# Kernel tuning notes

Hardware: AMD Instinct MI355X
Metric: run time of the kernel (lower is better)

The kernel has to match this reference:

```python
import jax, jax.numpy as jnp
import numpy as np

N_HEAD = 16


def setup_inputs() -> dict:
    key = jax.random.key(0)
    k1, k2, k3 = jax.random.split(key, 3)
    B, T, C = 2, 2048, 1024
    x = jax.random.normal(k1, (B, T, C), dtype=jnp.float32)
    Wqkv = jax.random.normal(k2, (C, 3 * C), dtype=jnp.float32) * 0.02
    bqkv = jnp.zeros((3 * C,), dtype=jnp.float32)
    Wproj = jax.random.normal(k3, (C, C), dtype=jnp.float32) * 0.02
    bproj = jnp.zeros((C,), dtype=jnp.float32)
    return {"x": x, "Wqkv": Wqkv, "bqkv": bqkv, "Wproj": Wproj, "bproj": bproj}


def reference(x, Wqkv, bqkv, Wproj, bproj):
    b, t, c = x.shape
    h = N_HEAD
    d = c // h  # head_dim
    # qkv projection, split into q,k,v per head: (b,t,3,h,d)
    qkv = (x @ Wqkv + bqkv).reshape(b, t, 3, h, d)
    q, k, v = qkv[:, :, 0], qkv[:, :, 1], qkv[:, :, 2]  # each (b,t,h,d)
    # Faithful quirk of original: n_state = head_dim // heads, scale = 1/sqrt(n_state)
    scale = jnp.float32(1.0 / np.sqrt(d // h))
    # attn_mode == 'all': dense non-causal attention
    w = jnp.einsum('bqhd,bkhd->bhqk', q, k)  # (b,h,t,t)
    w = jax.nn.softmax(w * scale, axis=-1)
    a = jnp.einsum('bhqk,bkhd->bqhd', w, v).reshape(b, t, c)
    return a @ Wproj + bproj
```

## Files before the change

### kernel.cpp

```cpp
#include <hip/hip_runtime.h>

typedef float floatx4 __attribute__((ext_vector_type(4)));
typedef float floatx16 __attribute__((ext_vector_type(16)));
typedef __bf16 bf16x8 __attribute__((ext_vector_type(8)));
typedef __bf16 bf16x4 __attribute__((ext_vector_type(4)));
typedef __bf16 bf16x2 __attribute__((ext_vector_type(2)));
typedef float floatx2 __attribute__((ext_vector_type(2)));

#define MFMA16 __builtin_amdgcn_mfma_f32_16x16x32_bf16
#define MFMA32 __builtin_amdgcn_mfma_f32_32x32x16_bf16

typedef const __attribute__((address_space(1))) void* gas_t;
typedef __attribute__((address_space(3))) void* las_t;
#define GLD16(g, l) __builtin_amdgcn_global_load_lds((gas_t)(g), (las_t)(l), 16, 0, 0)

static __device__ __forceinline__ unsigned short f2bf(float f) {
  union { float f; unsigned int u; } v; v.f = f;
  unsigned int r = v.u + 0x7fffu + ((v.u >> 16) & 1u);
  return (unsigned short)(r >> 16);
}

static __device__ __forceinline__ unsigned pk2(float a, float b) {
  floatx2 v; v[0] = a; v[1] = b;
  union { bf16x2 h; unsigned u; } u;
  u.h = __builtin_convertvector(v, bf16x2);
  return u.u;
}

static __device__ __forceinline__ void cast_transpose_tile(
    const float* __restrict__ in, unsigned short* __restrict__ out,
    int R, int C, int bx, int by) {
  const int r0 = by * 64, c0 = bx * 64;
  const int tid = threadIdx.x;
  __shared__ float tl[64][65];
  const int rr = tid >> 4, cc = (tid & 15) * 4;
#pragma unroll
  for (int i = 0; i < 4; ++i) {
    int row = rr + i * 16;
    float4 v = *(const float4*)(in + (size_t)(r0 + row) * C + c0 + cc);
    tl[row][cc] = v.x; tl[row][cc + 1] = v.y;
    tl[row][cc + 2] = v.z; tl[row][cc + 3] = v.w;
  }
  __syncthreads();
  const int cl = tid >> 2, rbase = (tid & 3) * 16;
  unsigned short o[16];
#pragma unroll
  for (int j = 0; j < 16; ++j) o[j] = f2bf(tl[rbase + j][cl]);
  unsigned short* dst = out + (size_t)(c0 + cl) * R + r0 + rbase;
  *(uint4*)dst = *(uint4*)o;
  *(uint4*)(dst + 8) = *(uint4*)(o + 8);
}

__global__ __launch_bounds__(256) void prologue_kernel(
    const float* __restrict__ x, unsigned short* __restrict__ Xb,
    const float* __restrict__ Wqkv, unsigned short* __restrict__ Wqkvt,
    const float* __restrict__ Wproj, unsigned short* __restrict__ Wprojt) {
  const int bid = blockIdx.x;
  if (bid < 4096) {
    int i = bid * 256 + threadIdx.x;
    float4 v = ((const float4*)x)[i];
    ushort4 o;
    o.x = f2bf(v.x); o.y = f2bf(v.y); o.z = f2bf(v.z); o.w = f2bf(v.w);
    ((ushort4*)Xb)[i] = o;
  } else if (bid < 4096 + 768) {
    int b2 = bid - 4096;
    cast_transpose_tile(Wqkv, Wqkvt, 1024, 3072, b2 % 48, b2 / 48);
  } else {
    int b3 = bid - 4096 - 768;
    cast_transpose_tile(Wproj, Wprojt, 1024, 1024, b3 % 16, b3 / 16);
  }
}

__global__ __launch_bounds__(256) void gemm_qkv(
    const unsigned short* __restrict__ A,
    const unsigned short* __restrict__ Bt,
    const float* __restrict__ bias,
    unsigned short* __restrict__ Q,
    unsigned short* __restrict__ Kc,
    unsigned short* __restrict__ Vt) {
  const int K = 1024;
  const int m0 = blockIdx.y * 128, n0 = blockIdx.x * 128;
  const int tid = threadIdx.x, w = tid >> 6, l = tid & 63;
  const int l16 = l & 15, lq = l >> 4;
  const int wm = w >> 1, wn = w & 1;
  const int which = n0 >> 10;

  __shared__ __align__(16) unsigned short SH[32768];

  floatx4 acc[4][4] = {};

  int sA[4], sB[4];
  unsigned ldso[4];
#pragma unroll
  for (int j = 0; j < 4; ++j) {
    int s = j * 256 + tid;
    int row = s >> 3, blk = (s & 7) ^ (row & 7);
    sA[j] = (m0 + row) * K + blk * 8;
    sB[j] = (n0 + row) * K + blk * 8;
    ldso[j] = (unsigned)(j * 256 + w * 64) * 8;
  }

#pragma unroll
  for (int j = 0; j < 4; ++j) {
    GLD16(A + sA[j], SH + ldso[j]);
    GLD16(Bt + sB[j], SH + 8192 + ldso[j]);
  }

  if (which == 2) {
    for (int k0 = 0; k0 < K; k0 += 64) {
      __syncthreads();
      const int cur = (k0 >> 6) & 1;
      if (k0 + 64 < K) {
        const int nxt = cur ^ 1;
#pragma unroll
        for (int j = 0; j < 4; ++j) {
          GLD16(A + sA[j] + k0 + 64, SH + nxt * 16384 + ldso[j]);
          GLD16(Bt + sB[j] + k0 + 64, SH + nxt * 16384 + 8192 + ldso[j]);
        }
      }
      const unsigned short* As = SH + cur * 16384;
      const unsigned short* Bs = SH + cur * 16384 + 8192;
#pragma unroll
      for (int kk = 0; kk < 2; ++kk) {
        bf16x8 af[4], bf[4];
#pragma unroll
        for (int mi = 0; mi < 4; ++mi) {
          int row = wm * 64 + mi * 16 + l16;
          int blk = (kk * 4 + lq) ^ (l16 & 7);
          af[mi] = *(const bf16x8*)(As + row * 64 + blk * 8);
        }
#pragma unroll
        for (int ni = 0; ni < 4; ++ni) {
          int row = wn * 64 + ni * 16 + l16;
          int blk = (kk * 4 + lq) ^ (l16 & 7);
          bf[ni] = *(const bf16x8*)(Bs + row * 64 + blk * 8);
        }
#pragma unroll
        for (int ni = 0; ni < 4; ++ni)
#pragma unroll
          for (int mi = 0; mi < 4; ++mi)
            acc[mi][ni] = MFMA16(af[mi], bf[ni], acc[mi][ni], 0, 0, 0);
      }
    }
    float bv[4];
#pragma unroll
    for (int ni = 0; ni < 4; ++ni) bv[ni] = bias[n0 + wn * 64 + ni * 16 + l16];
    __syncthreads();
    unsigned short* E = SH + w * 2304;
    const int bh = (m0 >> 11) * 16 + ((n0 & 1023) >> 6) + wn;
    const int tt0 = (m0 & 2047) + wm * 64;
    const int m8 = l & 7, bc = 16 * (m8 >> 1) + 4 * (m8 & 1);
#pragma unroll
    for (int p = 0; p < 2; ++p) {
#pragma unroll
      for (int n2 = 0; n2 < 2; ++n2) {
        int ni = p * 2 + n2;
#pragma unroll
        for (int mi = 0; mi < 4; ++mi) {
          floatx4 vv = acc[mi][ni] + bv[ni];
          *(bf16x4*)(E + (n2 * 16 + l16) * 72 + mi * 16 + lq * 4) =
              __builtin_convertvector(vv, bf16x4);
        }
      }
#pragma unroll
      for (int s = 0; s < 4; ++s) {
        int dl = s * 8 + (l >> 3);
        union { bf16x4 h[2]; bf16x8 v; } uu;
        uu.h[0] = *(const bf16x4*)(E + dl * 72 + bc);
        uu.h[1] = *(const bf16x4*)(E + dl * 72 + bc + 8);
        *(bf16x8*)(Vt + ((size_t)bh * 64 + p * 32 + dl) * 2048 + tt0 +
                   m8 * 8) = uu.v;
      }
    }
  } else {
    for (int k0 = 0; k0 < K; k0 += 64) {
      __syncthreads();
      const int cur = (k0 >> 6) & 1;
      if (k0 + 64 < K) {
        const int nxt = cur ^ 1;
#pragma unroll
        for (int j = 0; j < 4; ++j) {
          GLD16(A + sA[j] + k0 + 64, SH + nxt * 16384 + ldso[j]);
          GLD16(Bt + sB[j] + k0 + 64, SH + nxt * 16384 + 8192 + ldso[j]);
        }
      }
      const unsigned short* As = SH + cur * 16384;
      const unsigned short* Bs = SH + cur * 16384 + 8192;
#pragma unroll
      for (int kk = 0; kk < 2; ++kk) {
        bf16x8 af[4], bf[4];
#pragma unroll
        for (int mi = 0; mi < 4; ++mi) {
          int row = wm * 64 + mi * 16 + l16;
          int blk = (kk * 4 + lq) ^ (l16 & 7);
          af[mi] = *(const bf16x8*)(As + row * 64 + blk * 8);
        }
#pragma unroll
        for (int ni = 0; ni < 4; ++ni) {
          int row = wn * 64 + ni * 16 + l16;
          int blk = (kk * 4 + lq) ^ (l16 & 7);
          bf[ni] = *(const bf16x8*)(Bs + row * 64 + blk * 8);
        }
#pragma unroll
        for (int ni = 0; ni < 4; ++ni)
#pragma unroll
          for (int mi = 0; mi < 4; ++mi)
            acc[mi][ni] = MFMA16(bf[ni], af[mi], acc[mi][ni], 0, 0, 0);
      }
    }
    const float sc = (which == 0) ? 0.7213475204444817f : 1.0f;
    unsigned short* dst = (which == 0) ? Q : Kc;
    __syncthreads();
    unsigned short* E = SH + w * 2304;
    const int bh = (m0 >> 11) * 16 + ((n0 & 1023) >> 6) + wn;
    const size_t gbase = ((size_t)bh * 2048 + (m0 & 2047) + wm * 64) * 64;
#pragma unroll
    for (int p = 0; p < 2; ++p) {
#pragma unroll
      for (int m2 = 0; m2 < 2; ++m2) {
        int mi = p * 2 + m2;
#pragma unroll
        for (int ni = 0; ni < 4; ++ni) {
          int col0 = n0 + wn * 64 + ni * 16 + lq * 4;
          floatx4 bv = *(const floatx4*)(bias + col0);
          floatx4 vv = (acc[mi][ni] + bv) * sc;
          *(bf16x4*)(E + (m2 * 16 + l16) * 72 + ni * 16 + lq * 4) =
              __builtin_convertvector(vv, bf16x4);
        }
      }
#pragma unroll
      for (int s = 0; s < 4; ++s) {
        int rl = s * 8 + (l >> 3);
        bf16x8 vv = *(const bf16x8*)(E + rl * 72 + (l & 7) * 8);
        *(bf16x8*)(dst + gbase + (size_t)(p * 32 + rl) * 64 + (l & 7) * 8) =
            vv;
      }
    }
  }
}

__global__ __launch_bounds__(256, 2) void attn_kernel(
    const unsigned short* __restrict__ Q,
    const unsigned short* __restrict__ Kc,
    const unsigned short* __restrict__ Vt,
    unsigned short* __restrict__ AO) {
  const int T = 2048;
  const int bh = blockIdx.y, q0 = blockIdx.x * 128;
  const int tid = threadIdx.x, w = tid >> 6, l = tid & 63;
  const int r31 = l & 31, g = l >> 5;

  __shared__ __align__(16) unsigned short KVs[2][2][2][4096];

  bf16x8 qf[4];
  {
    const unsigned short* qr =
        Q + ((size_t)bh * T + q0 + w * 32 + r31) * 64 + g * 8;
#pragma unroll
    for (int ds = 0; ds < 4; ++ds) qf[ds] = *(const bf16x8*)(qr + ds * 16);
  }

  floatx16 o_acc[2] = {};
  float l_lane = 0.f;

  const unsigned short* kbase = Kc + (size_t)bh * T * 64;
  const unsigned short* vbase = Vt + (size_t)bh * 64 * T;
  int kro[2], vro[2];
  unsigned ldso[2];
#pragma unroll
  for (int j = 0; j < 2; ++j) {
    int s = j * 256 + tid;
    int row = s >> 3, blk = (s & 7) ^ (row & 7);
    kro[j] = row * 64 + blk * 8;
    vro[j] = row * T + blk * 8;
    ldso[j] = (unsigned)(j * 256 + (tid & 192)) * 8;
  }

#define STAGE_PERIOD(pp, nb)                                              \
  {                                                                       \
    _Pragma("unroll") for (int c2 = 0; c2 < 2; ++c2) {                    \
      const int c = (pp) * 2 + c2;                                        \
      _Pragma("unroll") for (int j = 0; j < 2; ++j) {                     \
        GLD16(kbase + c * 4096 + kro[j], &KVs[nb][0][c2][ldso[j]]);       \
        GLD16(vbase + c * 64 + vro[j], &KVs[nb][1][c2][ldso[j]]);         \
      }                                                                   \
    }                                                                     \
  }

  STAGE_PERIOD(0, 0);

  for (int p = 0; p < 16; ++p) {
    __syncthreads();
    if (p < 15) {
      const int nb = (p + 1) & 1;
      STAGE_PERIOD(p + 1, nb);
    }
    const int pb = p & 1;
#pragma unroll
    for (int c2 = 0; c2 < 2; ++c2) {
      const unsigned short* kb = &KVs[pb][0][c2][0];
      const unsigned short* vb = &KVs[pb][1][c2][0];

      bf16x8 pf[4];
#pragma unroll
      for (int kt = 0; kt < 2; ++kt) {
        const int row = kt * 32 + r31, rx = row & 7;
        const unsigned short* kr = kb + row * 64;
        floatx16 z = {};
#pragma unroll
        for (int ds = 0; ds < 4; ++ds)
          z = MFMA32(*(const bf16x8*)(kr + ((ds * 2 + g) ^ rx) * 8), qf[ds],
                     z, 0, 0, 0);

        float pe[16];
#pragma unroll
        for (int r = 0; r < 16; ++r) pe[r] = __builtin_amdgcn_exp2f(z[r]);
        l_lane += (((pe[0] + pe[1]) + (pe[2] + pe[3])) +
                   ((pe[4] + pe[5]) + (pe[6] + pe[7]))) +
                  (((pe[8] + pe[9]) + (pe[10] + pe[11])) +
                   ((pe[12] + pe[13]) + (pe[14] + pe[15])));
#pragma unroll
        for (int s2 = 0; s2 < 2; ++s2) {
          union { unsigned u[4]; bf16x8 v; } pu;
          pu.u[0] = pk2(pe[8 * s2 + 0], pe[8 * s2 + 1]);
          pu.u[1] = pk2(pe[8 * s2 + 2], pe[8 * s2 + 3]);
          pu.u[2] = pk2(pe[8 * s2 + 4], pe[8 * s2 + 5]);
          pu.u[3] = pk2(pe[8 * s2 + 6], pe[8 * s2 + 7]);
          pf[kt * 2 + s2] = pu.v;
        }
      }

#pragma unroll
      for (int dt = 0; dt < 2; ++dt) {
        const int row = dt * 32 + r31, rx = row & 7;
        const unsigned short* vr = vb + row * 64;
#pragma unroll
        for (int s = 0; s < 4; ++s) {
          bf16x8 vf = *(const bf16x8*)(vr + ((s * 2 + g) ^ rx) * 8);
          o_acc[dt] = MFMA32(vf, pf[s], o_acc[dt], 0, 0, 0);
        }
      }
    }
  }
#undef STAGE_PERIOD

  float ls = l_lane + __shfl_xor(l_lane, 32, 64);
  float inv = 1.0f / ls;
  const int b = bh >> 4, h = bh & 15;
  const int t = q0 + w * 32 + r31;
  unsigned short* ao = AO + ((size_t)b * 2048 + t) * 1024 + h * 64;
#pragma unroll
  for (int dt = 0; dt < 2; ++dt)
#pragma unroll
    for (int rq = 0; rq < 4; ++rq) {
      floatx4 ov;
      ov[0] = o_acc[dt][rq * 4 + 0]; ov[1] = o_acc[dt][rq * 4 + 1];
      ov[2] = o_acc[dt][rq * 4 + 2]; ov[3] = o_acc[dt][rq * 4 + 3];
      ov *= inv;
      *(bf16x4*)(ao + dt * 32 + rq * 8 + g * 4) =
          __builtin_convertvector(ov, bf16x4);
    }
}

__global__ __launch_bounds__(256) void gemm_proj(
    const unsigned short* __restrict__ A,
    const unsigned short* __restrict__ Bt,
    const float* __restrict__ bias,
    float* __restrict__ out) {
  const int K = 1024, N = 1024;
  const int m0 = blockIdx.y * 128, n0 = blockIdx.x * 64;
  const int tid = threadIdx.x, w = tid >> 6, l = tid & 63;
  const int l16 = l & 15, lq = l >> 4;

  __shared__ __align__(16) unsigned short SH[24576];

  floatx4 acc[2][4] = {};

  int sA[4], sB[2];
  unsigned ldsoA[4], ldsoB[2];
#pragma unroll
  for (int j = 0; j < 4; ++j) {
    int s = j * 256 + tid;
    int row = s >> 3, blk = (s & 7) ^ (row & 7);
    sA[j] = (m0 + row) * K + blk * 8;
    ldsoA[j] = (unsigned)(j * 256 + w * 64) * 8;
  }
#pragma unroll
  for (int j = 0; j < 2; ++j) {
    int s = j * 256 + tid;
    int row = s >> 3, blk = (s & 7) ^ (row & 7);
    sB[j] = (n0 + row) * K + blk * 8;
    ldsoB[j] = (unsigned)(j * 256 + w * 64) * 8;
  }

#pragma unroll
  for (int j = 0; j < 4; ++j) GLD16(A + sA[j], SH + ldsoA[j]);
#pragma unroll
  for (int j = 0; j < 2; ++j) GLD16(Bt + sB[j], SH + 8192 + ldsoB[j]);

  for (int k0 = 0; k0 < K; k0 += 64) {
    __syncthreads();
    const int cur = (k0 >> 6) & 1;
    if (k0 + 64 < K) {
      const int nxt = cur ^ 1;
#pragma unroll
      for (int j = 0; j < 4; ++j)
        GLD16(A + sA[j] + k0 + 64, SH + nxt * 12288 + ldsoA[j]);
#pragma unroll
      for (int j = 0; j < 2; ++j)
        GLD16(Bt + sB[j] + k0 + 64, SH + nxt * 12288 + 8192 + ldsoB[j]);
    }
    const unsigned short* As = SH + cur * 12288;
    const unsigned short* Bs = SH + cur * 12288 + 8192;
#pragma unroll
    for (int kk = 0; kk < 2; ++kk) {
      bf16x8 af[2], bf[4];
#pragma unroll
      for (int mi = 0; mi < 2; ++mi) {
        int row = w * 32 + mi * 16 + l16;
        int blk = (kk * 4 + lq) ^ (l16 & 7);
        af[mi] = *(const bf16x8*)(As + row * 64 + blk * 8);
      }
#pragma unroll
      for (int ni = 0; ni < 4; ++ni) {
        int row = ni * 16 + l16;
        int blk = (kk * 4 + lq) ^ (l16 & 7);
        bf[ni] = *(const bf16x8*)(Bs + row * 64 + blk * 8);
      }
#pragma unroll
      for (int ni = 0; ni < 4; ++ni)
#pragma unroll
        for (int mi = 0; mi < 2; ++mi)
          acc[mi][ni] = MFMA16(bf[ni], af[mi], acc[mi][ni], 0, 0, 0);
    }
  }

#pragma unroll
  for (int mi = 0; mi < 2; ++mi) {
    int t = m0 + w * 32 + mi * 16 + l16;
#pragma unroll
    for (int ni = 0; ni < 4; ++ni) {
      int col0 = n0 + ni * 16 + lq * 4;
      floatx4 bv = *(const floatx4*)(bias + col0);
      *(floatx4*)(out + (size_t)t * N + col0) = acc[mi][ni] + bv;
    }
  }
}

extern "C" void kernel_launch(void* const* d_in, const int* in_sizes, int n_in,
                              void* d_out, int out_size, void* d_ws,
                              size_t ws_size, hipStream_t stream) {
  const float* x     = (const float*)d_in[0];
  const float* Wqkv  = (const float*)d_in[1];
  const float* bqkv  = (const float*)d_in[2];
  const float* Wproj = (const float*)d_in[3];
  const float* bproj = (const float*)d_in[4];
  float* out = (float*)d_out;

  unsigned short* Xb     = (unsigned short*)d_ws;
  unsigned short* Wqkvt  = Xb + 4194304;
  unsigned short* Wprojt = Wqkvt + 3145728;
  unsigned short* Qb     = Wprojt + 1048576;
  unsigned short* Kb     = Qb + 4194304;
  unsigned short* Vtb    = Kb + 4194304;
  unsigned short* AOb    = Vtb + 4194304;

  prologue_kernel<<<5120, 256, 0, stream>>>(x, Xb, Wqkv, Wqkvt, Wproj, Wprojt);
  gemm_qkv<<<dim3(24, 32), 256, 0, stream>>>(Xb, Wqkvt, bqkv, Qb, Kb, Vtb);
  attn_kernel<<<dim3(16, 32), 256, 0, stream>>>(Qb, Kb, Vtb, AOb);
  gemm_proj<<<dim3(16, 32), 256, 0, stream>>>(AOb, Wprojt, bproj, out);
}
```

Before: 164.9 us.

## Double attention query tile per block to reuse K/V fragments across two query tiles

Each wave now handles 64 query rows (two 32-row tiles), so each block covers 256 queries. K fragments are loaded from LDS once and reused across both query tiles, and each V fragment feeds two MFMAs. This halves K/V staging traffic per query. The grid shrinks to 256 blocks with a remapped block index so blocks of the same head are spread out, and launch bounds drop to 1 block per SM. The cost is higher register pressure and only 256 blocks for 256 CUs, which may leave occupancy and latency hiding low.

Result: slower. 175.6 us (+6.5%).

```diff
diff --git a/kernel.cpp b/kernel.cpp
--- a/kernel.cpp
+++ b/kernel.cpp
@@ -239,28 +239,31 @@
   }
 }
 
-__global__ __launch_bounds__(256, 2) void attn_kernel(
+__global__ __launch_bounds__(256, 1) void attn_kernel(
     const unsigned short* __restrict__ Q,
     const unsigned short* __restrict__ Kc,
     const unsigned short* __restrict__ Vt,
     unsigned short* __restrict__ AO) {
   const int T = 2048;
-  const int bh = blockIdx.y, q0 = blockIdx.x * 128;
+  const int bid = blockIdx.x;
+  const int lin = (bid & 7) * 32 + (bid >> 3);
+  const int bh = lin >> 3, q0 = (lin & 7) * 256;
   const int tid = threadIdx.x, w = tid >> 6, l = tid & 63;
   const int r31 = l & 31, g = l >> 5;
 
   __shared__ __align__(16) unsigned short KVs[2][2][2][4096];
 
-  bf16x8 qf[4];
-  {
+  bf16x8 qf[2][4];
+#pragma unroll
+  for (int qt = 0; qt < 2; ++qt) {
     const unsigned short* qr =
-        Q + ((size_t)bh * T + q0 + w * 32 + r31) * 64 + g * 8;
-#pragma unroll
-    for (int ds = 0; ds < 4; ++ds) qf[ds] = *(const bf16x8*)(qr + ds * 16);
-  }
-
-  floatx16 o_acc[2] = {};
-  float l_lane = 0.f;
+        Q + ((size_t)bh * T + q0 + w * 64 + qt * 32 + r31) * 64 + g * 8;
+#pragma unroll
+    for (int ds = 0; ds < 4; ++ds) qf[qt][ds] = *(const bf16x8*)(qr + ds * 16);
+  }
+
+  floatx16 o_acc[2][2] = {};
+  float l_lane[2] = {0.f, 0.f};
 
   const unsigned short* kbase = Kc + (size_t)bh * T * 64;
   const unsigned short* vbase = Vt + (size_t)bh * 64 * T;
@@ -300,32 +303,42 @@
       const unsigned short* kb = &KVs[pb][0][c2][0];
       const unsigned short* vb = &KVs[pb][1][c2][0];
 
-      bf16x8 pf[4];
+      bf16x8 kf[2][4];
 #pragma unroll
       for (int kt = 0; kt < 2; ++kt) {
         const int row = kt * 32 + r31, rx = row & 7;
         const unsigned short* kr = kb + row * 64;
-        floatx16 z = {};
 #pragma unroll
         for (int ds = 0; ds < 4; ++ds)
-          z = MFMA32(*(const bf16x8*)(kr + ((ds * 2 + g) ^ rx) * 8), qf[ds],
-                     z, 0, 0, 0);
-
-        float pe[16];
-#pragma unroll
-        for (int r = 0; r < 16; ++r) pe[r] = __builtin_amdgcn_exp2f(z[r]);
-        l_lane += (((pe[0] + pe[1]) + (pe[2] + pe[3])) +
-                   ((pe[4] + pe[5]) + (pe[6] + pe[7]))) +
-                  (((pe[8] + pe[9]) + (pe[10] + pe[11])) +
-                   ((pe[12] + pe[13]) + (pe[14] + pe[15])));
-#pragma unroll
-        for (int s2 = 0; s2 < 2; ++s2) {
-          union { unsigned u[4]; bf16x8 v; } pu;
-          pu.u[0] = pk2(pe[8 * s2 + 0], pe[8 * s2 + 1]);
-          pu.u[1] = pk2(pe[8 * s2 + 2], pe[8 * s2 + 3]);
-          pu.u[2] = pk2(pe[8 * s2 + 4], pe[8 * s2 + 5]);
-          pu.u[3] = pk2(pe[8 * s2 + 6], pe[8 * s2 + 7]);
-          pf[kt * 2 + s2] = pu.v;
+          kf[kt][ds] = *(const bf16x8*)(kr + ((ds * 2 + g) ^ rx) * 8);
+      }
+
+      bf16x8 pf[2][4];
+#pragma unroll
+      for (int qt = 0; qt < 2; ++qt) {
+#pragma unroll
+        for (int kt = 0; kt < 2; ++kt) {
+          floatx16 z = {};
+#pragma unroll
+          for (int ds = 0; ds < 4; ++ds)
+            z = MFMA32(kf[kt][ds], qf[qt][ds], z, 0, 0, 0);
+
+          float pe[16];
+#pragma unroll
+          for (int r = 0; r < 16; ++r) pe[r] = __builtin_amdgcn_exp2f(z[r]);
+          l_lane[qt] += (((pe[0] + pe[1]) + (pe[2] + pe[3])) +
+                         ((pe[4] + pe[5]) + (pe[6] + pe[7]))) +
+                        (((pe[8] + pe[9]) + (pe[10] + pe[11])) +
+                         ((pe[12] + pe[13]) + (pe[14] + pe[15])));
+#pragma unroll
+          for (int s2 = 0; s2 < 2; ++s2) {
+            union { unsigned u[4]; bf16x8 v; } pu;
+            pu.u[0] = pk2(pe[8 * s2 + 0], pe[8 * s2 + 1]);
+            pu.u[1] = pk2(pe[8 * s2 + 2], pe[8 * s2 + 3]);
+            pu.u[2] = pk2(pe[8 * s2 + 4], pe[8 * s2 + 5]);
+            pu.u[3] = pk2(pe[8 * s2 + 6], pe[8 * s2 + 7]);
+            pf[qt][kt * 2 + s2] = pu.v;
+          }
         }
       }
 
@@ -336,29 +349,34 @@
 #pragma unroll
         for (int s = 0; s < 4; ++s) {
           bf16x8 vf = *(const bf16x8*)(vr + ((s * 2 + g) ^ rx) * 8);
-          o_acc[dt] = MFMA32(vf, pf[s], o_acc[dt], 0, 0, 0);
+#pragma unroll
+          for (int qt = 0; qt < 2; ++qt)
+            o_acc[qt][dt] = MFMA32(vf, pf[qt][s], o_acc[qt][dt], 0, 0, 0);
         }
       }
     }
   }
 #undef STAGE_PERIOD
 
-  float ls = l_lane + __shfl_xor(l_lane, 32, 64);
-  float inv = 1.0f / ls;
   const int b = bh >> 4, h = bh & 15;
-  const int t = q0 + w * 32 + r31;
-  unsigned short* ao = AO + ((size_t)b * 2048 + t) * 1024 + h * 64;
-#pragma unroll
-  for (int dt = 0; dt < 2; ++dt)
-#pragma unroll
-    for (int rq = 0; rq < 4; ++rq) {
-      floatx4 ov;
-      ov[0] = o_acc[dt][rq * 4 + 0]; ov[1] = o_acc[dt][rq * 4 + 1];
-      ov[2] = o_acc[dt][rq * 4 + 2]; ov[3] = o_acc[dt][rq * 4 + 3];
-      ov *= inv;
-      *(bf16x4*)(ao + dt * 32 + rq * 8 + g * 4) =
-          __builtin_convertvector(ov, bf16x4);
-    }
+#pragma unroll
+  for (int qt = 0; qt < 2; ++qt) {
+    float ls = l_lane[qt] + __shfl_xor(l_lane[qt], 32, 64);
+    float inv = 1.0f / ls;
+    const int t = q0 + w * 64 + qt * 32 + r31;
+    unsigned short* ao = AO + ((size_t)b * 2048 + t) * 1024 + h * 64;
+#pragma unroll
+    for (int dt = 0; dt < 2; ++dt)
+#pragma unroll
+      for (int rq = 0; rq < 4; ++rq) {
+        floatx4 ov;
+        ov[0] = o_acc[qt][dt][rq * 4 + 0]; ov[1] = o_acc[qt][dt][rq * 4 + 1];
+        ov[2] = o_acc[qt][dt][rq * 4 + 2]; ov[3] = o_acc[qt][dt][rq * 4 + 3];
+        ov *= inv;
+        *(bf16x4*)(ao + dt * 32 + rq * 8 + g * 4) =
+            __builtin_convertvector(ov, bf16x4);
+      }
+  }
 }
 
 __global__ __launch_bounds__(256) void gemm_proj(
@@ -466,6 +484,6 @@
 
   prologue_kernel<<<5120, 256, 0, stream>>>(x, Xb, Wqkv, Wqkvt, Wproj, Wprojt);
   gemm_qkv<<<dim3(24, 32), 256, 0, stream>>>(Xb, Wqkvt, bqkv, Qb, Kb, Vtb);
-  attn_kernel<<<dim3(16, 32), 256, 0, stream>>>(Qb, Kb, Vtb, AOb);
+  attn_kernel<<<256, 256, 0, stream>>>(Qb, Kb, Vtb, AOb);
   gemm_proj<<<dim3(16, 32), 256, 0, stream>>>(AOb, Wprojt, bproj, out);
 }
```

## Split attention KV range across wave pairs and combine partials in LDS

Applied to the files above, without the earlier changes.

Each attention block now covers 64 query rows instead of 128. Its four waves split into two KV halves, each pair handling 32 query rows over 1024 keys, and the two partial outputs and row sums are merged through shared memory at the end. The grid doubles to 1024 blocks, with a swizzled block index so that blocks sharing a head launch near each other. This raises the block count to fill more CUs, at the cost of loading K/V twice per query row set and adding an extra LDS reduction step.

Result: slower. 173.7 us (+5.4%).

```diff
diff --git a/kernel.cpp b/kernel.cpp
--- a/kernel.cpp
+++ b/kernel.cpp
@@ -245,16 +245,20 @@
     const unsigned short* __restrict__ Vt,
     unsigned short* __restrict__ AO) {
   const int T = 2048;
-  const int bh = blockIdx.y, q0 = blockIdx.x * 128;
+  const int bid = blockIdx.x;
+  const int lin = (bid & 7) * 128 + (bid >> 3);
+  const int bh = lin >> 5, q0 = (lin & 31) * 64;
   const int tid = threadIdx.x, w = tid >> 6, l = tid & 63;
   const int r31 = l & 31, g = l >> 5;
+  const int kh = w >> 1, wq = w & 1;
+  const int h128 = tid & 127;
 
   __shared__ __align__(16) unsigned short KVs[2][2][2][4096];
 
   bf16x8 qf[4];
   {
     const unsigned short* qr =
-        Q + ((size_t)bh * T + q0 + w * 32 + r31) * 64 + g * 8;
+        Q + ((size_t)bh * T + q0 + wq * 32 + r31) * 64 + g * 8;
 #pragma unroll
     for (int ds = 0; ds < 4; ++ds) qf[ds] = *(const bf16x8*)(qr + ds * 16);
   }
@@ -264,101 +268,118 @@
 
   const unsigned short* kbase = Kc + (size_t)bh * T * 64;
   const unsigned short* vbase = Vt + (size_t)bh * 64 * T;
-  int kro[2], vro[2];
-  unsigned ldso[2];
-#pragma unroll
-  for (int j = 0; j < 2; ++j) {
-    int s = j * 256 + tid;
+  int kro[4], vro[4];
+  unsigned ldso[4];
+#pragma unroll
+  for (int j = 0; j < 4; ++j) {
+    int s = j * 128 + h128;
     int row = s >> 3, blk = (s & 7) ^ (row & 7);
     kro[j] = row * 64 + blk * 8;
     vro[j] = row * T + blk * 8;
-    ldso[j] = (unsigned)(j * 256 + (tid & 192)) * 8;
-  }
-
-#define STAGE_PERIOD(pp, nb)                                              \
-  {                                                                       \
-    _Pragma("unroll") for (int c2 = 0; c2 < 2; ++c2) {                    \
-      const int c = (pp) * 2 + c2;                                        \
-      _Pragma("unroll") for (int j = 0; j < 2; ++j) {                     \
-        GLD16(kbase + c * 4096 + kro[j], &KVs[nb][0][c2][ldso[j]]);       \
-        GLD16(vbase + c * 64 + vro[j], &KVs[nb][1][c2][ldso[j]]);         \
-      }                                                                   \
-    }                                                                     \
-  }
-
-  STAGE_PERIOD(0, 0);
-
-  for (int p = 0; p < 16; ++p) {
+    ldso[j] = (unsigned)(j * 128 + (h128 & 64)) * 8;
+  }
+
+  {
+    const int c0 = kh * 16;
+#pragma unroll
+    for (int j = 0; j < 4; ++j) {
+      GLD16(kbase + c0 * 4096 + kro[j], &KVs[0][kh][0][ldso[j]]);
+      GLD16(vbase + c0 * 64 + vro[j], &KVs[1][kh][0][ldso[j]]);
+    }
+  }
+
+  for (int it = 0; it < 16; ++it) {
     __syncthreads();
-    if (p < 15) {
-      const int nb = (p + 1) & 1;
-      STAGE_PERIOD(p + 1, nb);
-    }
-    const int pb = p & 1;
-#pragma unroll
-    for (int c2 = 0; c2 < 2; ++c2) {
-      const unsigned short* kb = &KVs[pb][0][c2][0];
-      const unsigned short* vb = &KVs[pb][1][c2][0];
-
-      bf16x8 pf[4];
-#pragma unroll
-      for (int kt = 0; kt < 2; ++kt) {
-        const int row = kt * 32 + r31, rx = row & 7;
-        const unsigned short* kr = kb + row * 64;
-        floatx16 z = {};
-#pragma unroll
-        for (int ds = 0; ds < 4; ++ds)
-          z = MFMA32(*(const bf16x8*)(kr + ((ds * 2 + g) ^ rx) * 8), qf[ds],
-                     z, 0, 0, 0);
-
-        float pe[16];
-#pragma unroll
-        for (int r = 0; r < 16; ++r) pe[r] = __builtin_amdgcn_exp2f(z[r]);
-        l_lane += (((pe[0] + pe[1]) + (pe[2] + pe[3])) +
-                   ((pe[4] + pe[5]) + (pe[6] + pe[7]))) +
-                  (((pe[8] + pe[9]) + (pe[10] + pe[11])) +
-                   ((pe[12] + pe[13]) + (pe[14] + pe[15])));
-#pragma unroll
-        for (int s2 = 0; s2 < 2; ++s2) {
-          union { unsigned u[4]; bf16x8 v; } pu;
-          pu.u[0] = pk2(pe[8 * s2 + 0], pe[8 * s2 + 1]);
-          pu.u[1] = pk2(pe[8 * s2 + 2], pe[8 * s2 + 3]);
-          pu.u[2] = pk2(pe[8 * s2 + 4], pe[8 * s2 + 5]);
-          pu.u[3] = pk2(pe[8 * s2 + 6], pe[8 * s2 + 7]);
-          pf[kt * 2 + s2] = pu.v;
-        }
-      }
-
-#pragma unroll
-      for (int dt = 0; dt < 2; ++dt) {
-        const int row = dt * 32 + r31, rx = row & 7;
-        const unsigned short* vr = vb + row * 64;
-#pragma unroll
-        for (int s = 0; s < 4; ++s) {
-          bf16x8 vf = *(const bf16x8*)(vr + ((s * 2 + g) ^ rx) * 8);
-          o_acc[dt] = MFMA32(vf, pf[s], o_acc[dt], 0, 0, 0);
-        }
-      }
-    }
-  }
-#undef STAGE_PERIOD
-
-  float ls = l_lane + __shfl_xor(l_lane, 32, 64);
-  float inv = 1.0f / ls;
-  const int b = bh >> 4, h = bh & 15;
-  const int t = q0 + w * 32 + r31;
-  unsigned short* ao = AO + ((size_t)b * 2048 + t) * 1024 + h * 64;
-#pragma unroll
-  for (int dt = 0; dt < 2; ++dt)
-#pragma unroll
-    for (int rq = 0; rq < 4; ++rq) {
-      floatx4 ov;
-      ov[0] = o_acc[dt][rq * 4 + 0]; ov[1] = o_acc[dt][rq * 4 + 1];
-      ov[2] = o_acc[dt][rq * 4 + 2]; ov[3] = o_acc[dt][rq * 4 + 3];
-      ov *= inv;
-      *(bf16x4*)(ao + dt * 32 + rq * 8 + g * 4) =
-          __builtin_convertvector(ov, bf16x4);
-    }
+    if (it + 1 < 16) {
+      const int cn = kh * 16 + it + 1, nb = (it + 1) & 1;
+#pragma unroll
+      for (int j = 0; j < 4; ++j) {
+        GLD16(kbase + cn * 4096 + kro[j], &KVs[0][kh][nb][ldso[j]]);
+        GLD16(vbase + cn * 64 + vro[j], &KVs[1][kh][nb][ldso[j]]);
+      }
+    }
+    const unsigned short* kb = &KVs[0][kh][it & 1][0];
+    const unsigned short* vb = &KVs[1][kh][it & 1][0];
+
+    bf16x8 pf[4];
+#pragma unroll
+    for (int kt = 0; kt < 2; ++kt) {
+      const int row = kt * 32 + r31, rx = row & 7;
+      const unsigned short* kr = kb + row * 64;
+      floatx16 z = {};
+#pragma unroll
+      for (int ds = 0; ds < 4; ++ds)
+        z = MFMA32(*(const bf16x8*)(kr + ((ds * 2 + g) ^ rx) * 8), qf[ds], z,
+                   0, 0, 0);
+
+      float pe[16];
+#pragma unroll
+      for (int r = 0; r < 16; ++r) pe[r] = __builtin_amdgcn_exp2f(z[r]);
+      l_lane += (((pe[0] + pe[1]) + (pe[2] + pe[3])) +
+                 ((pe[4] + pe[5]) + (pe[6] + pe[7]))) +
+                (((pe[8] + pe[9]) + (pe[10] + pe[11])) +
+                 ((pe[12] + pe[13]) + (pe[14] + pe[15])));
+#pragma unroll
+      for (int s2 = 0; s2 < 2; ++s2) {
+        union { unsigned u[4]; bf16x8 v; } pu;
+        pu.u[0] = pk2(pe[8 * s2 + 0], pe[8 * s2 + 1]);
+        pu.u[1] = pk2(pe[8 * s2 + 2], pe[8 * s2 + 3]);
+        pu.u[2] = pk2(pe[8 * s2 + 4], pe[8 * s2 + 5]);
+        pu.u[3] = pk2(pe[8 * s2 + 6], pe[8 * s2 + 7]);
+        pf[kt * 2 + s2] = pu.v;
+      }
+    }
+
+#pragma unroll
+    for (int dt = 0; dt < 2; ++dt) {
+      const int row = dt * 32 + r31, rx = row & 7;
+      const unsigned short* vr = vb + row * 64;
+#pragma unroll
+      for (int s = 0; s < 4; ++s) {
+        bf16x8 vf = *(const bf16x8*)(vr + ((s * 2 + g) ^ rx) * 8);
+        o_acc[dt] = MFMA32(vf, pf[s], o_acc[dt], 0, 0, 0);
+      }
+    }
+  }
+
+  __syncthreads();
+  float* oex = (float*)&KVs[0][0][0][0];
+  float* Lex = oex + 128 * 36;
+  if (kh == 1) {
+    float* r = oex + (wq * 64 + l) * 36;
+#pragma unroll
+    for (int dt = 0; dt < 2; ++dt)
+#pragma unroll
+      for (int rq = 0; rq < 4; ++rq) {
+        floatx4 ov;
+        ov[0] = o_acc[dt][rq * 4 + 0]; ov[1] = o_acc[dt][rq * 4 + 1];
+        ov[2] = o_acc[dt][rq * 4 + 2]; ov[3] = o_acc[dt][rq * 4 + 3];
+        *(floatx4*)(r + dt * 16 + rq * 4) = ov;
+      }
+    Lex[wq * 64 + l] = l_lane;
+  }
+  __syncthreads();
+  if (kh == 0) {
+    const float* r = oex + (wq * 64 + l) * 36;
+    float ls = l_lane + Lex[wq * 64 + l];
+    ls += __shfl_xor(ls, 32, 64);
+    float inv = 1.0f / ls;
+    const int b = bh >> 4, h = bh & 15;
+    const int t = q0 + wq * 32 + r31;
+    unsigned short* ao = AO + ((size_t)b * 2048 + t) * 1024 + h * 64;
+#pragma unroll
+    for (int dt = 0; dt < 2; ++dt)
+#pragma unroll
+      for (int rq = 0; rq < 4; ++rq) {
+        floatx4 ov;
+        ov[0] = o_acc[dt][rq * 4 + 0]; ov[1] = o_acc[dt][rq * 4 + 1];
+        ov[2] = o_acc[dt][rq * 4 + 2]; ov[3] = o_acc[dt][rq * 4 + 3];
+        ov += *(const floatx4*)(r + dt * 16 + rq * 4);
+        ov *= inv;
+        *(bf16x4*)(ao + dt * 32 + rq * 8 + g * 4) =
+            __builtin_convertvector(ov, bf16x4);
+      }
+  }
 }
 
 __global__ __launch_bounds__(256) void gemm_proj(
@@ -466,6 +487,6 @@
 
   prologue_kernel<<<5120, 256, 0, stream>>>(x, Xb, Wqkv, Wqkvt, Wproj, Wprojt);
   gemm_qkv<<<dim3(24, 32), 256, 0, stream>>>(Xb, Wqkvt, bqkv, Qb, Kb, Vtb);
-  attn_kernel<<<dim3(16, 32), 256, 0, stream>>>(Qb, Kb, Vtb, AOb);
+  attn_kernel<<<1024, 256, 0, stream>>>(Qb, Kb, Vtb, AOb);
   gemm_proj<<<dim3(16, 32), 256, 0, stream>>>(AOb, Wprojt, bproj, out);
 }
```
